# Kernel tuning notes

Measured on AMD Instinct MI355X. Metric: run time of the kernel, lower is better.

Reference implementation:

```python
import jax, jax.numpy as jnp
import numpy as np

N, L, H, E, FE = 32, 128, 16, 256, 4  # batch, seq_len, heads, embed_size, forward_expansion
EPS = 1e-5
NEG_SLOPE = 0.01


def _mask_positions(qe):
    # zero entries where j < L-1-i (torch: triu(ones,1).flip(1) == 1)
    Ld = qe.shape[-1]
    i = jnp.arange(Ld)[:, None]
    j = jnp.arange(Ld)[None, :]
    return jnp.where(j >= (Ld - 1 - i), qe, jnp.zeros((), qe.dtype))


def _skew(qe):
    # pad last dim on the left, reinterpret, drop first row -> relative skew
    n, h, Ld, _ = qe.shape
    p = jnp.pad(qe, ((0, 0), (0, 0), (0, 0), (1, 0)))
    return p.reshape(n, h, Ld + 1, Ld)[:, :, 1:, :]


def _batchnorm(x, gamma, beta):
    # BatchNorm1d(C=L*H) over (N, C, E): normalize over batch and embed dims
    mean = jnp.mean(x, axis=(0, 2), keepdims=True)
    var = jnp.var(x, axis=(0, 2), keepdims=True)
    return (x - mean) * jax.lax.rsqrt(var + EPS) * gamma[None, :, None] + beta[None, :, None]


def _leaky(x):
    return jnp.where(x >= 0, x, NEG_SLOPE * x)


def setup_inputs() -> dict:
    key = jax.random.key(0)
    ks = jax.random.split(key, 16)
    s_e = 1.0 / np.sqrt(E)
    d = {
        "x": jax.random.normal(ks[0], (N, L * H, E, 1), dtype=jnp.float32),
        "Wq": jax.random.normal(ks[1], (E, E), dtype=jnp.float32) * s_e,
        "bq": jnp.zeros((E,), jnp.float32),
        "Wk": jax.random.normal(ks[2], (E, E), dtype=jnp.float32) * s_e,
        "bk": jnp.zeros((E,), jnp.float32),
        "Wv": jax.random.normal(ks[3], (E, E), dtype=jnp.float32) * s_e,
        "bv": jnp.zeros((E,), jnp.float32),
        "Erel": jax.random.normal(ks[4], (H, L, E), dtype=jnp.float32),
        "Wo": jax.random.normal(ks[5], (E, E), dtype=jnp.float32) * s_e,
        "bo": jnp.zeros((E,), jnp.float32),
        "g1": jnp.ones((L * H,), jnp.float32),
        "be1": jnp.zeros((L * H,), jnp.float32),
        "g2": jnp.ones((L * H,), jnp.float32),
        "be2": jnp.zeros((L * H,), jnp.float32),
        "W1": jax.random.normal(ks[6], (E, FE * E), dtype=jnp.float32) * s_e,
        "b1": jnp.zeros((FE * E,), jnp.float32),
        "W2": jax.random.normal(ks[7], (FE * E, E), dtype=jnp.float32) * (1.0 / np.sqrt(FE * E)),
        "b2": jnp.zeros((E,), jnp.float32),
        "Wenc": jax.random.normal(ks[8], (E, E), dtype=jnp.float32) * s_e,
        "benc": jnp.zeros((E,), jnp.float32),
    }
    return d


def reference(x, Wq, bq, Wk, bk, Wv, bv, Erel, Wo, bo, g1, be1, g2, be2, W1, b1, W2, b2, Wenc, benc):
    xs = x[:, :, :, 0]  # (N, L*H, E)
    q = (xs @ Wq + bq).reshape(N, L, H, E)
    k = (xs @ Wk + bk).reshape(N, L, H, E)
    v = (xs @ Wv + bv).reshape(N, L, H, E)
    # relative-position skew term (Music-Transformer style)
    QE = jnp.einsum('nlhe,hme->nhlm', q, Erel)       # (N,H,L,L)
    S = _skew(_mask_positions(QE))                   # (N,H,L,L)
    qk = jnp.einsum('nqhe,nkhe->nhqk', q, k)         # (N,H,L,L)
    att = jax.nn.softmax(qk / jnp.sqrt(jnp.float32(E)), axis=-1) + S
    z = jnp.einsum('nhql,nlhe->nqhe', att, v).reshape(N, L * H, E)
    z = z @ Wo + bo
    h1 = _batchnorm(z + xs, g1, be1)
    ff = _leaky(h1 @ W1 + b1) @ W2 + b2
    out = _batchnorm(ff + h1, g2, be2)
    return out @ Wenc + benc
```

## Files before the change

### kernel.cpp

```cpp
#include <hip/hip_runtime.h>
#include <hip/hip_bf16.h>

using u16 = unsigned short;
typedef __attribute__((ext_vector_type(8))) short bf16x8;
typedef __attribute__((ext_vector_type(4))) float f32x4;

static constexpr float EPS_ = 1e-5f;
static constexpr float NEG_ = 0.01f;

__device__ __forceinline__ float bf2f(u16 u) { return __uint_as_float(((unsigned)u) << 16); }
__device__ __forceinline__ u16 f2bf(float f) {
    union { __hip_bfloat16 h; u16 u; } c; c.h = __float2bfloat16(f); return c.u;
}

#define MFMA16(a, b, c) __builtin_amdgcn_mfma_f32_16x16x32_bf16(a, b, c, 0, 0, 0)

__device__ __forceinline__ void gload16(const u16* g, u16* l) {
    __builtin_amdgcn_global_load_lds(
        (__attribute__((address_space(1))) void*)(u16*)g,
        (__attribute__((address_space(3))) void*)l, 16, 0, 0);
}

__device__ __forceinline__ int xswz(int nwg) {
    const int b = blockIdx.x;
    return (b & 7) * (nwg >> 3) + (b >> 3);
}

template<int K>
__device__ __forceinline__ void core256(
    const u16* __restrict__ Ag, int lda,
    const u16* __restrict__ Bg, int ldb,
    u16* SH, f32x4 acc[8][4])
{
    const int tid = threadIdx.x;
    const int w = tid >> 6, lane = tid & 63;
    const int g = lane >> 4, r = lane & 15;
    const int wr = w >> 2, wc = w & 3;
    const int sx = r & 7;
    constexpr int NT = K / 64;

    #pragma unroll
    for (int i = 0; i < 8; i++)
        #pragma unroll
        for (int j = 0; j < 4; j++)
            acc[i][j] = (f32x4){0.f, 0.f, 0.f, 0.f};

    auto stage = [&](int d, int kt, int rnd) {
        const int j = rnd & 3;
        const int u = j * 512 + w * 64 + lane;
        const int row = u >> 3;
        const int c8 = (u & 7) ^ (row & 7);
        u16* ldst = SH + d * 32768 + (rnd < 4 ? 0 : 16384) + (j * 512 + w * 64) * 8;
        const u16* src = (rnd < 4 ? Ag + (size_t)row * lda : Bg + (size_t)row * ldb)
                         + kt + c8 * 8;
        gload16(src, ldst);
    };

    #pragma unroll
    for (int rnd = 0; rnd < 8; ++rnd) stage(0, 0, rnd);
    asm volatile("s_waitcnt vmcnt(0)" ::: "memory");
    __builtin_amdgcn_s_barrier();
    __builtin_amdgcn_sched_barrier(0);

    for (int t = 0; t < NT; ++t) {
        const int d = t & 1;
        const u16* Asd = SH + d * 32768;
        const u16* Bsd = Asd + 16384;
        #pragma unroll
        for (int q = 0; q < 4; ++q) {
            const int mh = q >> 1, nh = q & 1;
            if (t + 1 < NT) {
                stage(d ^ 1, (t + 1) * 64, q * 2);
                stage(d ^ 1, (t + 1) * 64, q * 2 + 1);
            }
            bf16x8 af[2][4], bfr[2][2];
            #pragma unroll
            for (int kk = 0; kk < 2; ++kk) {
                const int co = ((kk * 4 + g) ^ sx) * 8;
                #pragma unroll
                for (int f = 0; f < 4; ++f)
                    af[kk][f] = *(const bf16x8*)(Asd + (wr*128 + mh*64 + f*16 + r) * 64 + co);
                #pragma unroll
                for (int e = 0; e < 2; ++e)
                    bfr[kk][e] = *(const bf16x8*)(Bsd + (wc*64 + (nh*2+e)*16 + r) * 64 + co);
            }
            __builtin_amdgcn_s_setprio(1);
            #pragma unroll
            for (int kk = 0; kk < 2; ++kk)
                #pragma unroll
                for (int f = 0; f < 4; ++f)
                    #pragma unroll
                    for (int e = 0; e < 2; ++e)
                        acc[mh*4+f][nh*2+e] =
                            MFMA16(af[kk][f], bfr[kk][e], acc[mh*4+f][nh*2+e]);
            __builtin_amdgcn_s_setprio(0);
            if (q == 3) asm volatile("s_waitcnt vmcnt(0)" ::: "memory");
            __builtin_amdgcn_s_barrier();
            __builtin_amdgcn_sched_barrier(0);
        }
    }
}

template<int K, int NN, int MODE>
__global__ __launch_bounds__(512, 2) void gemm256_k(
    const u16* __restrict__ A, const u16* __restrict__ Bt,
    const float* __restrict__ bias, const u16* __restrict__ res,
    const float2* __restrict__ rp, const float* __restrict__ cs,
    void* __restrict__ outv)
{
    __shared__ __align__(16) u16 SH[65536];
    constexpr int NB = NN / 256;
    const int f = xswz(256 * NB);
    const int m0 = (f / NB) * 256, n0 = (f % NB) * 256;

    f32x4 acc[8][4];
    core256<K>(A + (size_t)m0 * K, K, Bt + (size_t)n0 * K, K, SH, acc);

    const int tid = threadIdx.x;
    const int w = tid >> 6, lane = tid & 63;
    const int g = lane >> 4, r = lane & 15;
    const int wr = w >> 2, wc = w & 3;

    if constexpr (MODE == 3) {
        float* out = (float*)outv;
        #pragma unroll
        for (int fn = 0; fn < 4; ++fn) {
            const int n = n0 + wc * 64 + fn * 16 + r;
            const float bv = bias[n], cv = cs[n];
            #pragma unroll
            for (int fm = 0; fm < 8; ++fm)
                #pragma unroll
                for (int reg = 0; reg < 4; ++reg) {
                    const int m = m0 + wr * 128 + fm * 16 + g * 4 + reg;
                    const float2 pp = rp[m & 2047];
                    out[(size_t)m * NN + n] = pp.x * acc[fm][fn][reg] + pp.y * cv + bv;
                }
        }
        return;
    }
    u16* out = (u16*)outv;
    #pragma unroll
    for (int h = 0; h < 2; ++h) {
        if (wr == h) {
            #pragma unroll
            for (int fm = 0; fm < 8; ++fm)
                #pragma unroll
                for (int fn = 0; fn < 4; ++fn) {
                    const int col = wc * 64 + fn * 16 + r;
                    const float bv = bias[n0 + col];
                    #pragma unroll
                    for (int reg = 0; reg < 4; ++reg) {
                        const int rl = fm * 16 + g * 4 + reg;
                        float v = acc[fm][fn][reg];
                        if constexpr (MODE == 1) {
                            const float2 pp = rp[(m0 + h * 128 + rl) & 2047];
                            v = pp.x * v + pp.y * cs[n0 + col] + bv;
                            v = v >= 0.f ? v : NEG_ * v;
                        } else {
                            v += bv;
                        }
                        SH[rl * 264 + col] = f2bf(v);
                    }
                }
        }
        __builtin_amdgcn_s_barrier();
        #pragma unroll
        for (int p = 0; p < 8; ++p) {
            const int ck = p * 512 + tid;
            const int rl = ck >> 5, cc = ck & 31;
            const int m = m0 + h * 128 + rl;
            bf16x8 v = *(const bf16x8*)(SH + rl * 264 + cc * 8);
            if constexpr (MODE == 0) {
                const bf16x8 rv = *(const bf16x8*)(res + (size_t)m * NN + n0 + cc * 8);
                #pragma unroll
                for (int j = 0; j < 8; ++j)
                    v[j] = (short)f2bf(bf2f((u16)v[j]) + bf2f((u16)rv[j]));
            }
            if constexpr (MODE == 2) {
                const float2 pp = rp[m & 2047];
                const bf16x8 rv = *(const bf16x8*)(res + (size_t)m * NN + n0 + cc * 8);
                #pragma unroll
                for (int j = 0; j < 8; ++j)
                    v[j] = (short)f2bf(bf2f((u16)v[j]) + pp.x * bf2f((u16)rv[j]) + pp.y);
            }
            *(bf16x8*)(out + (size_t)m * NN + n0 + cc * 8) = v;
        }
        __builtin_amdgcn_s_barrier();
    }
}

__global__ __launch_bounds__(512, 2) void qkv256_k(
    const u16* __restrict__ xbf, const u16* __restrict__ Wqkvt,
    const float* __restrict__ bq, const float* __restrict__ bk,
    const float* __restrict__ bv,
    u16* __restrict__ qo, u16* __restrict__ ko, u16* __restrict__ vo)
{
    __shared__ __align__(16) u16 SH[65536];
    const int f = xswz(768);
    const int m0 = (f / 3) * 256;
    const int which = f % 3;
    const float* bias = which == 0 ? bq : (which == 1 ? bk : bv);

    f32x4 acc[8][4];
    core256<256>(xbf + (size_t)m0 * 256, 256,
                 Wqkvt + (size_t)which * 65536, 256, SH, acc);

    const int tid = threadIdx.x;
    const int w = tid >> 6, lane = tid & 63;
    const int g = lane >> 4, r = lane & 15;
    const int wr = w >> 2, wc = w & 3;
    const int nn = m0 >> 11;

    if (which < 2) {
        u16* out = which == 0 ? qo : ko;
        #pragma unroll
        for (int h = 0; h < 2; ++h) {
            if (wr == h) {
                #pragma unroll
                for (int fm = 0; fm < 8; ++fm)
                    #pragma unroll
                    for (int fn = 0; fn < 4; ++fn) {
                        const int col = wc * 64 + fn * 16 + r;
                        const float bv4 = bias[col];
                        #pragma unroll
                        for (int reg = 0; reg < 4; ++reg) {
                            const int rl = fm * 16 + g * 4 + reg;
                            SH[rl * 264 + col] = f2bf(acc[fm][fn][reg] + bv4);
                        }
                    }
            }
            __builtin_amdgcn_s_barrier();
            #pragma unroll
            for (int p = 0; p < 8; ++p) {
                const int ck = p * 512 + tid;
                const int rl = ck >> 5, cc = ck & 31;
                const int m = m0 + h * 128 + rl;
                const int l = (m & 2047) >> 4, hh = m & 15;
                const bf16x8 v = *(const bf16x8*)(SH + rl * 264 + cc * 8);
                *(bf16x8*)(out + ((size_t)(nn * 16 + hh) * 128 + l) * 256 + cc * 8) = v;
            }
            __builtin_amdgcn_s_barrier();
        }
    } else {
        #pragma unroll
        for (int h = 0; h < 2; ++h) {
            if (wr == h) {
                #pragma unroll
                for (int fm = 0; fm < 8; ++fm)
                    #pragma unroll
                    for (int fn = 0; fn < 4; ++fn) {
                        const int col = wc * 64 + fn * 16 + r;
                        const float bv4 = bias[col];
                        #pragma unroll
                        for (int reg = 0; reg < 4; ++reg) {
                            const int rl = fm * 16 + g * 4 + reg;
                            SH[col * 136 + ((rl & 15) * 8 | (rl >> 4))] =
                                f2bf(acc[fm][fn][reg] + bv4);
                        }
                    }
            }
            __builtin_amdgcn_s_barrier();
            const int l0 = ((m0 + h * 128) & 2047) >> 4;
            #pragma unroll
            for (int p = 0; p < 8; ++p) {
                const int ck = p * 512 + tid;
                const int e = ck >> 4, hh = ck & 15;
                const bf16x8 v = *(const bf16x8*)(SH + e * 136 + hh * 8);
                *(bf16x8*)(vo + ((size_t)(nn * 16 + hh) * 256 + e) * 128 + l0) = v;
            }
            __builtin_amdgcn_s_barrier();
        }
    }
}

__device__ __forceinline__ void lds_core(
    const u16* __restrict__ Ag, int lda,
    const u16* __restrict__ Bg, int ldb, int K,
    u16* As, u16* Bs, f32x4 acc[4][4])
{
    const int tid = threadIdx.x;
    const int w = tid >> 6, lane = tid & 63;
    const int g = lane >> 4, r = lane & 15;
    const int wm = (w >> 1) * 64, wn = (w & 1) * 64;

    for (int kt = 0; kt < K; kt += 64) {
        #pragma unroll
        for (int j = 0; j < 4; j++) {
            const int ubase = (w * 4 + j) * 64;
            const int u = ubase + lane;
            const int row = u >> 3, cb = (u & 7) * 8;
            gload16(Ag + (size_t)row * lda + kt + cb, As + ubase * 8);
            gload16(Bg + (size_t)row * ldb + kt + cb, Bs + ubase * 8);
        }
        __syncthreads();
        #pragma unroll
        for (int kk = 0; kk < 2; kk++) {
            bf16x8 af[4], bfr[4];
            #pragma unroll
            for (int f = 0; f < 4; f++) {
                af[f]  = *(const bf16x8*)(As + (wm + f * 16 + r) * 64 + kk * 32 + g * 8);
                bfr[f] = *(const bf16x8*)(Bs + (wn + f * 16 + r) * 64 + kk * 32 + g * 8);
            }
            #pragma unroll
            for (int i = 0; i < 4; i++)
                #pragma unroll
                for (int j = 0; j < 4; j++)
                    acc[i][j] = MFMA16(af[i], bfr[j], acc[i][j]);
        }
        __syncthreads();
    }
}

template<typename OutF>
__device__ __forceinline__ void epi_store128(
    u16* Cs, f32x4 (&acc)[4][4], float scale, OutF outp)
{
    const int tid = threadIdx.x;
    const int w = tid >> 6, lane = tid & 63;
    const int g = lane >> 4, r = lane & 15;
    const int mb = (w >> 1) * 64, nb = (w & 1) * 64;

    #pragma unroll
    for (int fn = 0; fn < 4; fn++) {
        const int col = nb + fn * 16 + r;
        #pragma unroll
        for (int fm = 0; fm < 4; fm++)
            #pragma unroll
            for (int reg = 0; reg < 4; reg++) {
                const int row = mb + fm * 16 + g * 4 + reg;
                Cs[row * 136 + col] = f2bf(acc[fm][fn][reg] * scale);
            }
    }
    __syncthreads();
    #pragma unroll
    for (int p = 0; p < 8; p++) {
        const int ck = p * 256 + tid;
        const int row = ck >> 4, cc = ck & 15;
        const bf16x8 v = *(const bf16x8*)(Cs + row * 136 + cc * 8);
        *(bf16x8*)outp(row, cc) = v;
    }
}

__global__ __launch_bounds__(256) void qkqe_k(
    const u16* __restrict__ q, const u16* __restrict__ kc,
    const u16* __restrict__ erel, u16* __restrict__ out)
{
    __shared__ __align__(16) u16 SH[17408];
    u16* As = SH; u16* Bs = SH + 8192;
    const int f = xswz(1024);
    const int b = f >> 1, h = b & 15;
    const int n0 = (f & 1) * 128;
    const u16* Ag = q + (size_t)b * 128 * 256;
    const u16* Bg = (n0 == 0) ? (kc + (size_t)b * 128 * 256)
                              : (erel + (size_t)h * 128 * 256);

    f32x4 acc[4][4];
    #pragma unroll
    for (int i = 0; i < 4; i++)
        #pragma unroll
        for (int j = 0; j < 4; j++) acc[i][j] = (f32x4){0.f,0.f,0.f,0.f};
    lds_core(Ag, 256, Bg, 256, 256, As, Bs, acc);

    const float scale = (n0 == 0) ? 0.0625f : 1.0f;
    epi_store128(SH, acc, scale,
        [&](int row, int cc) -> u16* {
            return out + ((size_t)b * 128 + row) * 256 + n0 + cc * 8;
        });
}

__global__ __launch_bounds__(256) void softmax_k(
    const u16* __restrict__ qk, u16* __restrict__ att)
{
    const int r = blockIdx.x * 4 + (threadIdx.x >> 6);
    const int lane = threadIdx.x & 63;
    const int i = r & 127;
    const u16* row = qk + (size_t)r * 256;
    const float x0 = bf2f(row[lane]), x1 = bf2f(row[lane + 64]);
    float mx = fmaxf(x0, x1);
    #pragma unroll
    for (int o = 32; o; o >>= 1) mx = fmaxf(mx, __shfl_xor(mx, o));
    const float e0 = __expf(x0 - mx), e1 = __expf(x1 - mx);
    float s = e0 + e1;
    #pragma unroll
    for (int o = 32; o; o >>= 1) s += __shfl_xor(s, o);
    const float rinv = 1.0f / s;
    const float s0 = (lane <= i) ? bf2f(row[128 + 127 - i + lane]) : 0.f;
    const float s1 = (lane + 64 <= i) ? bf2f(row[128 + 127 - i + lane + 64]) : 0.f;
    att[(size_t)r * 128 + lane] = f2bf(e0 * rinv + s0);
    att[(size_t)r * 128 + lane + 64] = f2bf(e1 * rinv + s1);
}

__global__ __launch_bounds__(256) void av_k(
    const u16* __restrict__ att, const u16* __restrict__ vT,
    u16* __restrict__ zc)
{
    __shared__ __align__(16) u16 SH[17408];
    u16* As = SH; u16* Bs = SH + 8192;
    const int f = xswz(1024);
    const int b = f >> 1;
    const int n0 = (f & 1) * 128;
    const u16* Ag = att + (size_t)b * 128 * 128;
    const u16* Bg = vT + (size_t)b * 256 * 128 + (size_t)n0 * 128;

    f32x4 acc[4][4];
    #pragma unroll
    for (int i = 0; i < 4; i++)
        #pragma unroll
        for (int j = 0; j < 4; j++) acc[i][j] = (f32x4){0.f,0.f,0.f,0.f};
    lds_core(Ag, 128, Bg, 128, 128, As, Bs, acc);

    const int nn = b >> 4, hh = b & 15;
    epi_store128(SH, acc, 1.f,
        [&](int row, int cc) -> u16* {
            return zc + ((size_t)(nn * 2048 + row * 16 + hh)) * 256 + n0 + cc * 8;
        });
}

__global__ __launch_bounds__(256) void cvt_k(const float* __restrict__ in,
                                             u16* __restrict__ out) {
    const size_t i8 = ((size_t)blockIdx.x * 256 + threadIdx.x) * 8;
    const float4 lo = *(const float4*)(in + i8);
    const float4 hi = *(const float4*)(in + i8 + 4);
    ushort4 o0, o1;
    o0.x = f2bf(lo.x); o0.y = f2bf(lo.y); o0.z = f2bf(lo.z); o0.w = f2bf(lo.w);
    o1.x = f2bf(hi.x); o1.y = f2bf(hi.y); o1.z = f2bf(hi.z); o1.w = f2bf(hi.w);
    *(ushort4*)(out + i8) = o0;
    *(ushort4*)(out + i8 + 4) = o1;
}

__global__ __launch_bounds__(256) void prep_w_k(
    const float* __restrict__ Wq, const float* __restrict__ Wk,
    const float* __restrict__ Wv, const float* __restrict__ Wo,
    const float* __restrict__ Wenc, const float* __restrict__ W1,
    const float* __restrict__ W2, const float* __restrict__ Erel,
    u16* __restrict__ Wqkvt, u16* __restrict__ Wot, u16* __restrict__ Wenct,
    u16* __restrict__ W1t, u16* __restrict__ W2t, u16* __restrict__ Erelb,
    float* __restrict__ cs1, float* __restrict__ csE)
{
    const int bid = blockIdx.x, tid = threadIdx.x;
    if (bid < 1280) {
        const int jb = bid >> 8;
        const int t = ((bid & 255) << 8) | tid;
        const int n = t >> 8, k = t & 255;
        const float* src = jb == 0 ? Wq : jb == 1 ? Wk : jb == 2 ? Wv
                         : jb == 3 ? Wo : Wenc;
        const u16 v = f2bf(src[(k << 8) + n]);
        if (jb < 3)       Wqkvt[jb * 65536 + t] = v;
        else if (jb == 3) Wot[t] = v;
        else              Wenct[t] = v;
    } else if (bid < 2304) {
        const int t = ((bid - 1280) << 8) | tid;
        const int n = t >> 8, k = t & 255;
        W1t[t] = f2bf(W1[(k << 10) + n]);
    } else if (bid < 3328) {
        const int t = ((bid - 2304) << 8) | tid;
        const int n = t >> 10, k = t & 1023;
        W2t[t] = f2bf(W2[(k << 8) + n]);
    } else if (bid < 5376) {
        const int t = ((bid - 3328) << 8) | tid;
        Erelb[t] = f2bf(Erel[t]);
    } else {
        const int n = (bid - 5376) * 256 + tid;
        if (n < 1024) {
            float s = 0.f;
            for (int k = 0; k < 256; ++k) s += bf2f(f2bf(W1[(size_t)k * 1024 + n]));
            cs1[n] = s;
        } else {
            const int n2 = n - 1024;
            float s = 0.f;
            for (int k = 0; k < 256; ++k) s += bf2f(f2bf(Wenc[(size_t)k * 256 + n2]));
            csE[n2] = s;
        }
    }
}

__global__ __launch_bounds__(256) void bnstats_k(
    const u16* __restrict__ x, const float* __restrict__ g,
    const float* __restrict__ be, float2* __restrict__ params)
{
    const int c = blockIdx.x, tid = threadIdx.x;
    float s = 0.f, s2 = 0.f;
    #pragma unroll 4
    for (int n = 0; n < 32; n++) {
        const float v = bf2f(x[((size_t)n * 2048 + c) * 256 + tid]);
        s += v; s2 += v * v;
    }
    #pragma unroll
    for (int o = 32; o; o >>= 1) { s += __shfl_xor(s, o); s2 += __shfl_xor(s2, o); }
    __shared__ float rs[4], rs2[4];
    const int w = tid >> 6;
    if ((tid & 63) == 0) { rs[w] = s; rs2[w] = s2; }
    __syncthreads();
    if (tid == 0) {
        s  = rs[0] + rs[1] + rs[2] + rs[3];
        s2 = rs2[0] + rs2[1] + rs2[2] + rs2[3];
        const float mean = s / 8192.f;
        const float var = s2 / 8192.f - mean * mean;
        const float a = g[c] * rsqrtf(var + EPS_);
        params[c] = make_float2(a, be[c] - mean * a);
    }
}

extern "C" void kernel_launch(void* const* d_in, const int* in_sizes, int n_in,
                              void* d_out, int out_size, void* d_ws, size_t ws_size,
                              hipStream_t stream)
{
    const float* x    = (const float*)d_in[0];
    const float* Wq   = (const float*)d_in[1];
    const float* bq   = (const float*)d_in[2];
    const float* Wk   = (const float*)d_in[3];
    const float* bk   = (const float*)d_in[4];
    const float* Wv   = (const float*)d_in[5];
    const float* bv   = (const float*)d_in[6];
    const float* Erel = (const float*)d_in[7];
    const float* Wo   = (const float*)d_in[8];
    const float* bo   = (const float*)d_in[9];
    const float* g1   = (const float*)d_in[10];
    const float* be1  = (const float*)d_in[11];
    const float* g2   = (const float*)d_in[12];
    const float* be2  = (const float*)d_in[13];
    const float* W1   = (const float*)d_in[14];
    const float* b1   = (const float*)d_in[15];
    const float* W2   = (const float*)d_in[16];
    const float* b2   = (const float*)d_in[17];
    const float* Wenc = (const float*)d_in[18];
    const float* benc = (const float*)d_in[19];

    char* ws = (char*)d_ws;
    const size_t MB = 1ull << 20;
    const size_t KB = 1024;
    u16* xbf   = (u16*)(ws + 0 * MB);
    u16* h2pre = (u16*)(ws + 32 * MB);
    u16* qb    = (u16*)(ws + 32 * MB);
    u16* kb    = (u16*)(ws + 64 * MB);
    u16* vT    = (u16*)(ws + 96 * MB);
    u16* qkb   = (u16*)(ws + 128 * MB);
    u16* attb  = (u16*)(ws + 160 * MB);
    u16* ff1   = (u16*)(ws + 64 * MB);
    u16* zc    = (u16*)(ws + 176 * MB);
    u16* h1pre = (u16*)(ws + 208 * MB);
    u16* Wqkvt = (u16*)(ws + 240 * MB);
    u16* Wot   = (u16*)(ws + 240 * MB + 512 * KB);
    u16* Wenct = (u16*)(ws + 240 * MB + 640 * KB);
    u16* W1t   = (u16*)(ws + 240 * MB + 768 * KB);
    u16* W2t   = (u16*)(ws + 240 * MB + 1280 * KB);
    u16* Erelb = (u16*)(ws + 240 * MB + 1792 * KB);
    float2* p1 = (float2*)(ws + 243 * MB);
    float2* p2 = (float2*)(ws + 243 * MB + 16 * KB);
    float* cs1 = (float*)(ws + 243 * MB + 32 * KB);
    float* csE = (float*)(ws + 243 * MB + 40 * KB);

    const dim3 b256(256), b512(512);

    cvt_k<<<dim3(8192), b256, 0, stream>>>(x, xbf);
    prep_w_k<<<dim3(5381), b256, 0, stream>>>(Wq, Wk, Wv, Wo, Wenc, W1, W2, Erel,
                                              Wqkvt, Wot, Wenct, W1t, W2t, Erelb,
                                              cs1, csE);

    qkv256_k<<<dim3(768), b512, 0, stream>>>(xbf, Wqkvt, bq, bk, bv, qb, kb, vT);
    qkqe_k<<<dim3(1024), b256, 0, stream>>>(qb, kb, Erelb, qkb);
    softmax_k<<<dim3(16384), b256, 0, stream>>>(qkb, attb);
    av_k<<<dim3(1024), b256, 0, stream>>>(attb, vT, zc);
    gemm256_k<256, 256, 0><<<dim3(256), b512, 0, stream>>>(
        zc, Wot, bo, xbf, nullptr, nullptr, h1pre);

    bnstats_k<<<dim3(2048), b256, 0, stream>>>(h1pre, g1, be1, p1);

    gemm256_k<256, 1024, 1><<<dim3(1024), b512, 0, stream>>>(
        h1pre, W1t, b1, nullptr, p1, cs1, ff1);
    gemm256_k<1024, 256, 2><<<dim3(256), b512, 0, stream>>>(
        ff1, W2t, b2, h1pre, p1, nullptr, h2pre);

    bnstats_k<<<dim3(2048), b256, 0, stream>>>(h2pre, g2, be2, p2);
    gemm256_k<256, 256, 3><<<dim3(256), b512, 0, stream>>>(
        h2pre, Wenct, benc, nullptr, p2, csE, (float*)d_out);
}
```

Baseline: 357.3 us.

## Restructure 256x256 GEMM core into triple-buffered K=32 pipeline with less LDS

The shared 256-tile GEMM core now uses 32-wide K slices with three LDS buffers and prefetches two steps ahead, instead of double-buffered 64-wide slices. Global loads are interleaved between two MFMA half-phases, and the wait drops to vmcnt(4) so one stage stays in flight. LDS per block falls from 128KB to 96KB. The XOR swizzle is removed, which may bring back LDS bank conflicts on the 64-byte rows. Barriers are added before the epilogues that reuse shared memory.

```diff
diff --git a/kernel.cpp b/kernel.cpp
--- a/kernel.cpp
+++ b/kernel.cpp
@@ -36,8 +36,7 @@
     const int w = tid >> 6, lane = tid & 63;
     const int g = lane >> 4, r = lane & 15;
     const int wr = w >> 2, wc = w & 3;
-    const int sx = r & 7;
-    constexpr int NT = K / 64;
+    constexpr int NT = K / 32;
 
     #pragma unroll
     for (int i = 0; i < 8; i++)
@@ -45,59 +44,63 @@
         for (int j = 0; j < 4; j++)
             acc[i][j] = (f32x4){0.f, 0.f, 0.f, 0.f};
 
-    auto stage = [&](int d, int kt, int rnd) {
-        const int j = rnd & 3;
-        const int u = j * 512 + w * 64 + lane;
-        const int row = u >> 3;
-        const int c8 = (u & 7) ^ (row & 7);
-        u16* ldst = SH + d * 32768 + (rnd < 4 ? 0 : 16384) + (j * 512 + w * 64) * 8;
-        const u16* src = (rnd < 4 ? Ag + (size_t)row * lda : Bg + (size_t)row * ldb)
-                         + kt + c8 * 8;
-        gload16(src, ldst);
+    auto stage = [&](int buf, int kt, int rnd) {
+        const int part = rnd & 1, isB = rnd >> 1;
+        const int u = part * 512 + tid;
+        const int row = u >> 2, sc = u & 3;
+        const u16* src = (isB ? Bg + (size_t)row * ldb : Ag + (size_t)row * lda)
+                         + kt + sc * 8;
+        gload16(src, SH + buf * 16384 + isB * 8192 + u * 8);
     };
 
     #pragma unroll
-    for (int rnd = 0; rnd < 8; ++rnd) stage(0, 0, rnd);
-    asm volatile("s_waitcnt vmcnt(0)" ::: "memory");
+    for (int rnd = 0; rnd < 4; ++rnd) stage(0, 0, rnd);
+    #pragma unroll
+    for (int rnd = 0; rnd < 4; ++rnd) stage(1, 32, rnd);
+    asm volatile("s_waitcnt vmcnt(4)" ::: "memory");
     __builtin_amdgcn_s_barrier();
     __builtin_amdgcn_sched_barrier(0);
 
+    int cur = 0;
     for (int t = 0; t < NT; ++t) {
-        const int d = t & 1;
-        const u16* Asd = SH + d * 32768;
-        const u16* Bsd = Asd + 16384;
-        #pragma unroll
-        for (int q = 0; q < 4; ++q) {
-            const int mh = q >> 1, nh = q & 1;
-            if (t + 1 < NT) {
-                stage(d ^ 1, (t + 1) * 64, q * 2);
-                stage(d ^ 1, (t + 1) * 64, q * 2 + 1);
-            }
-            bf16x8 af[2][4], bfr[2][2];
-            #pragma unroll
-            for (int kk = 0; kk < 2; ++kk) {
-                const int co = ((kk * 4 + g) ^ sx) * 8;
-                #pragma unroll
-                for (int f = 0; f < 4; ++f)
-                    af[kk][f] = *(const bf16x8*)(Asd + (wr*128 + mh*64 + f*16 + r) * 64 + co);
-                #pragma unroll
-                for (int e = 0; e < 2; ++e)
-                    bfr[kk][e] = *(const bf16x8*)(Bsd + (wc*64 + (nh*2+e)*16 + r) * 64 + co);
-            }
-            __builtin_amdgcn_s_setprio(1);
-            #pragma unroll
-            for (int kk = 0; kk < 2; ++kk)
-                #pragma unroll
-                for (int f = 0; f < 4; ++f)
-                    #pragma unroll
-                    for (int e = 0; e < 2; ++e)
-                        acc[mh*4+f][nh*2+e] =
-                            MFMA16(af[kk][f], bfr[kk][e], acc[mh*4+f][nh*2+e]);
-            __builtin_amdgcn_s_setprio(0);
-            if (q == 3) asm volatile("s_waitcnt vmcnt(0)" ::: "memory");
-            __builtin_amdgcn_s_barrier();
-            __builtin_amdgcn_sched_barrier(0);
-        }
+        const u16* Ab = SH + cur * 16384;
+        const u16* Bb = Ab + 8192;
+        const bool pf = (t + 2 < NT);
+        const int nb = cur + 2 >= 3 ? cur - 1 : cur + 2;
+
+        if (pf) { stage(nb, (t + 2) * 32, 0); stage(nb, (t + 2) * 32, 1); }
+        bf16x8 bfr[4], af[4];
+        #pragma unroll
+        for (int fn = 0; fn < 4; ++fn)
+            bfr[fn] = *(const bf16x8*)(Bb + (wc * 64 + fn * 16 + r) * 32 + g * 8);
+        #pragma unroll
+        for (int f = 0; f < 4; ++f)
+            af[f] = *(const bf16x8*)(Ab + (wr * 128 + f * 16 + r) * 32 + g * 8);
+        __builtin_amdgcn_s_setprio(1);
+        #pragma unroll
+        for (int f = 0; f < 4; ++f)
+            #pragma unroll
+            for (int fn = 0; fn < 4; ++fn)
+                acc[f][fn] = MFMA16(af[f], bfr[fn], acc[f][fn]);
+        __builtin_amdgcn_s_setprio(0);
+
+        if (pf) { stage(nb, (t + 2) * 32, 2); stage(nb, (t + 2) * 32, 3); }
+        #pragma unroll
+        for (int f = 0; f < 4; ++f)
+            af[f] = *(const bf16x8*)(Ab + (wr * 128 + 64 + f * 16 + r) * 32 + g * 8);
+        __builtin_amdgcn_s_setprio(1);
+        #pragma unroll
+        for (int f = 0; f < 4; ++f)
+            #pragma unroll
+            for (int fn = 0; fn < 4; ++fn)
+                acc[4 + f][fn] = MFMA16(af[f], bfr[fn], acc[4 + f][fn]);
+        __builtin_amdgcn_s_setprio(0);
+
+        if (pf) asm volatile("s_waitcnt vmcnt(4)" ::: "memory");
+        else    asm volatile("s_waitcnt vmcnt(0)" ::: "memory");
+        __builtin_amdgcn_s_barrier();
+        __builtin_amdgcn_sched_barrier(0);
+        cur = cur + 1 == 3 ? 0 : cur + 1;
     }
 }
 
@@ -108,7 +111,7 @@
     const float2* __restrict__ rp, const float* __restrict__ cs,
     void* __restrict__ outv)
 {
-    __shared__ __align__(16) u16 SH[65536];
+    __shared__ __align__(16) u16 SH[49152];
     constexpr int NB = NN / 256;
     const int f = xswz(256 * NB);
     const int m0 = (f / NB) * 256, n0 = (f % NB) * 256;
@@ -138,6 +141,7 @@
         }
         return;
     }
+    __syncthreads();
     u16* out = (u16*)outv;
     #pragma unroll
     for (int h = 0; h < 2; ++h) {
@@ -195,7 +199,7 @@
     const float* __restrict__ bv,
     u16* __restrict__ qo, u16* __restrict__ ko, u16* __restrict__ vo)
 {
-    __shared__ __align__(16) u16 SH[65536];
+    __shared__ __align__(16) u16 SH[49152];
     const int f = xswz(768);
     const int m0 = (f / 3) * 256;
     const int which = f % 3;
@@ -211,6 +215,7 @@
     const int wr = w >> 2, wc = w & 3;
     const int nn = m0 >> 11;
 
+    __syncthreads();
     if (which < 2) {
         u16* out = which == 0 ? qo : ko;
         #pragma unroll
@@ -362,6 +367,7 @@
     lds_core(Ag, 256, Bg, 256, 256, As, Bs, acc);
 
     const float scale = (n0 == 0) ? 0.0625f : 1.0f;
+    __syncthreads();
     epi_store128(SH, acc, scale,
         [&](int row, int cc) -> u16* {
             return out + ((size_t)b * 128 + row) * 256 + n0 + cc * 8;
@@ -410,6 +416,7 @@
     lds_core(Ag, 128, Bg, 128, 128, As, Bs, acc);
 
     const int nn = b >> 4, hh = b & 15;
+    __syncthreads();
     epi_store128(SH, acc, 1.f,
         [&](int row, int cc) -> u16* {
             return zc + ((size_t)(nn * 2048 + row * 16 + hh)) * 256 + n0 + cc * 8;
```

After: 360.1 us. No clear change (+0.8%).
